# Kernel optimization log

Measured on AMD Instinct MI355X. Metric: run time of the kernel, lower is better.

The kernel has to match this reference:

```python
import jax, jax.numpy as jnp
import numpy as np

IN_FEATURES = 1024
OUT_FEATURES = 64
DEGREE = 3
NUM_KNOTS = 10
BATCH = 8192
K0 = NUM_KNOTS + DEGREE  # number of basis columns / control points per edge


def b_spline_basis(x, knots, degree):
    """Vectorized Cox-de Boor recursion.
    x: (..., ) values in [0,1]; knots: (K0+1,).
    Returns (..., K0) basis; last `degree` columns are zero-padded (matches
    control_points width of num_knots+degree as in the original module).
    """
    t = knots
    n0 = t.shape[0] - 1  # = K0 degree-0 intervals
    xe = x[..., None]
    basis = ((xe >= t[:-1]) & (xe < t[1:])).astype(x.dtype)  # (..., K0)
    for p in range(1, degree + 1):
        ti = t[: n0 - p]
        tip = t[p:n0]
        ti1 = t[1 : n0 - p + 1]
        tip1 = t[p + 1 : n0 + 1]
        d1 = jnp.where(tip - ti > 0, tip - ti, jnp.ones_like(ti))
        d2 = jnp.where(tip1 - ti1 > 0, tip1 - ti1, jnp.ones_like(ti1))
        left = jnp.where(tip - ti > 0, (xe - ti) / d1, 0.0) * basis[..., : n0 - p]
        right = jnp.where(tip1 - ti1 > 0, (tip1 - xe) / d2, 0.0) * basis[..., 1 : n0 - p + 1]
        new = left + right
        pad = jnp.zeros(x.shape + (p,), x.dtype)
        basis = jnp.concatenate([new, pad], axis=-1)
    return basis


def setup_inputs() -> dict:
    key = jax.random.key(0)
    k1, k2 = jax.random.split(key)
    x = jax.random.uniform(k1, (BATCH, IN_FEATURES), dtype=jnp.float32)
    knots = jnp.linspace(0.0, 1.0, NUM_KNOTS + DEGREE + 1, dtype=jnp.float32)
    control_points = jax.random.normal(k2, (OUT_FEATURES, IN_FEATURES, K0), dtype=jnp.float32)
    return {"x": x, "knots": knots, "control_points": control_points}


def reference(x, knots, control_points):
    # basis: (B, in, K0) computed once per input feature (original recomputes
    # it out_features times inside a double loop -- same math, fused here).
    basis = b_spline_basis(x, knots, DEGREE)
    # outputs[b, o] = sum_j sum_k basis[b, j, k] * control_points[o, j, k]
    return jnp.einsum("bjk,ojk->bo", basis, control_points)
```

## Files before the change

kernel.cpp:

```cpp
#include <hip/hip_runtime.h>
#include <hip/hip_bf16.h>
#include <stdint.h>

#define IN_F   1024
#define OUT_F  64
#define BATCH  8192
#define BM     256
#define NTHR   256
#define JSPLIT 32
#define JPB    (IN_F / JSPLIT)
#define JC     4
#define NCH    (JPB / JC)
#define BT_B   (JC * 2048)
#define TBL_B  (14 * 32 * 48)
#define XSTG_B (BM * JPB * 4)
#define LDS_T  (TBL_B + XSTG_B + 2 * BT_B)
#define OUTSZ  (BATCH * OUT_F)

typedef __attribute__((ext_vector_type(8)))  short short8;
typedef __attribute__((ext_vector_type(16))) float f32x16;

__device__ __forceinline__ void gll16(const void* g, void* l) {
    __builtin_amdgcn_global_load_lds(
        (const __attribute__((address_space(1))) uint32_t*)g,
        (__attribute__((address_space(3))) uint32_t*)l,
        16, 0, 0);
}

__global__ void kan_prep(const float* __restrict__ cp, __hip_bfloat16* __restrict__ bt) {
    int j = blockIdx.x * 4 + (threadIdx.x >> 6);
    int o = threadIdx.x & 63;
    const float* src = cp + ((size_t)o * IN_F + j) * 13;
    float v[16];
#pragma unroll
    for (int k = 0; k < 10; ++k) v[k] = src[k];
#pragma unroll
    for (int k = 10; k < 16; ++k) v[k] = 0.0f;
    __hip_bfloat16* dst = bt + (size_t)j * 1024;
#pragma unroll
    for (int kh = 0; kh < 2; ++kh)
#pragma unroll
        for (int e = 0; e < 8; ++e)
            dst[kh * 512 + o * 8 + e] = __float2bfloat16(v[kh * 8 + e]);
}

template<bool PART>
__launch_bounds__(NTHR, 2)
__global__ void kan_main(const float* __restrict__ x,
                         const __hip_bfloat16* __restrict__ bt,
                         void* __restrict__ outp) {
    __shared__ __attribute__((aligned(16))) char lds[LDS_T];

    const int tid   = threadIdx.x;
    const int w     = tid >> 6;
    const int lane  = tid & 63;
    const int l31   = lane & 31;
    const int khalf = lane >> 5;

    const int r0 = blockIdx.x * BM;
    const int j0 = blockIdx.y * JPB;

    const char* btg = (const char*)bt + (size_t)j0 * 2048 + (size_t)tid * 16;
    const char* xgt = (const char*)(x + (size_t)(r0 + tid) * IN_F + j0);
    const int   wofs = w << 10;

#pragma unroll
    for (int p = 0; p < JPB / 4; ++p)
        gll16(xgt + p * 16, lds + TBL_B + p * 4096 + wofs);

#define STAGE_BT(ch, bi) do {                                     \
        char* base_ = lds + TBL_B + XSTG_B + (bi) * BT_B;         \
        const char* gb_ = btg + (size_t)(ch) * BT_B;              \
        gll16(gb_,        base_ + wofs);                          \
        gll16(gb_ + 4096, base_ + 4096 + wofs);                   \
    } while (0)

    STAGE_BT(0, 0);
    STAGE_BT(1, 1);

    for (int e = tid; e < 14 * 32; e += NTHR) {
        const int m = e >> 5, u5 = e & 31;
        const float uu = (u5 + 0.5f) * (1.0f / 32.0f);
        const float u2 = uu * uu;
        const float omu = 1.0f - uu;
        const float o2 = omu * omu;
        const float B3 = u2 * (uu * (1.0f / 6.0f));
        const float B0 = o2 * (omu * (1.0f / 6.0f));
        const float B1 = __builtin_fmaf(u2, __builtin_fmaf(uu, 0.5f, -1.0f), 2.0f / 3.0f);
        const float B2 = 1.0f - B0 - B1 - B3;
        uint32_t P01, P23;
        asm("v_cvt_pk_bf16_f32 %0, %1, %2" : "=v"(P01) : "v"(B0), "v"(B1));
        asm("v_cvt_pk_bf16_f32 %0, %1, %2" : "=v"(P23) : "v"(B2), "v"(B3));
        const uint64_t V = ((uint64_t)P23 << 32) | (uint64_t)P01;
#pragma unroll
        for (int h = 0; h < 2; ++h) {
            const int c0 = 48 + (h << 7);
            const int p = (m << 4) - c0;
            const uint64_t sl = V << ((uint32_t)p & 63);
            const uint64_t sr = V >> ((uint32_t)(-p) & 63);
            const uint64_t t0 = (p < 0) ? sr : sl;
            const uint64_t q0 = ((uint32_t)(p + 63) < 127u) ? t0 : 0ull;
            const uint64_t t1 = (p < 64) ? sr : sl;
            const uint64_t q1 = ((uint32_t)(p - 16) < 112u) ? t1 : 0ull;
            uint64_t* d = (uint64_t*)(lds + e * 48 + h * 16);
            d[0] = q0; d[1] = q1;
        }
    }

#define AFRAG(xv) ({                                              \
        const float t416_ = (xv) * 416.0f;           \
        const int i_ = (int)t416_;                 \
        const int s_ = ((i_ << 1) + i_) << 4;         \
        *(const short8*)(lds + s_ + (khalf << 4)); })

#define COMPUTE(ch, bi) do {                                                  \
        const char* base = lds + TBL_B + XSTG_B + (bi) * BT_B;                \
        float xa0[4], xa1[4];                                                 \
        const char* xr = lds + TBL_B + (ch) * 4096 + (((w << 6) + l31) << 4); \
        *(float4*)xa0 = *(const float4*)(xr);              \
        *(float4*)xa1 = *(const float4*)(xr + 512);     \
        const char* bbb = base + (khalf << 10) + l31 * 16;                    \
        _Pragma("unroll")                                                     \
        for (int jl = 0; jl < JC; ++jl) {                                     \
            const short8 b0 = *(const short8*)(bbb + jl * 2048);              \
            const short8 b1 = *(const short8*)(bbb + jl * 2048 + 512);        \
            const short8 a0 = AFRAG(xa0[jl]);                                 \
            const short8 a1 = AFRAG(xa1[jl]);                                 \
            acc00 = __builtin_amdgcn_mfma_f32_32x32x16_bf16(a0, b0, acc00, 0, 0, 0); \
            acc01 = __builtin_amdgcn_mfma_f32_32x32x16_bf16(a0, b1, acc01, 0, 0, 0); \
            acc10 = __builtin_amdgcn_mfma_f32_32x32x16_bf16(a1, b0, acc10, 0, 0, 0); \
            acc11 = __builtin_amdgcn_mfma_f32_32x32x16_bf16(a1, b1, acc11, 0, 0, 0); \
        }                                                                     \
    } while (0)

    f32x16 acc00, acc01, acc10, acc11;
#pragma unroll
    for (int i = 0; i < 16; ++i) {
        acc00[i] = 0.0f; acc01[i] = 0.0f; acc10[i] = 0.0f; acc11[i] = 0.0f;
    }

    __syncthreads();

    int cur = 0;
#pragma unroll 1
    for (int ch = 0; ch < NCH; ++ch) {
        if (ch >= 2) {
            asm volatile("s_waitcnt vmcnt(2)" ::: "memory");
            __builtin_amdgcn_s_barrier();
            __builtin_amdgcn_sched_barrier(0);
        }
        COMPUTE(ch, cur);
        if (ch + 2 < NCH) {
            __builtin_amdgcn_s_barrier();
            __builtin_amdgcn_sched_barrier(0);
            STAGE_BT(ch + 2, cur);
        }
        cur ^= 1;
    }
#undef STAGE_BT
#undef AFRAG
#undef COMPUTE

    if (PART) {
        __hip_bfloat16* op = (__hip_bfloat16*)outp + (size_t)blockIdx.y * OUTSZ;
#pragma unroll
        for (int r = 0; r < 16; ++r) {
            const int crow = (r & 3) + 8 * (r >> 2) + 4 * khalf;
            __hip_bfloat16* p0 = op + (size_t)(r0 + (w << 6) + crow) * OUT_F;
            __hip_bfloat16* p1 = p0 + 32 * OUT_F;
            p0[l31]      = __float2bfloat16(acc00[r]);
            p0[l31 + 32] = __float2bfloat16(acc01[r]);
            p1[l31]      = __float2bfloat16(acc10[r]);
            p1[l31 + 32] = __float2bfloat16(acc11[r]);
        }
    } else {
        float* op = (float*)outp;
#pragma unroll
        for (int r = 0; r < 16; ++r) {
            const int crow = (r & 3) + 8 * (r >> 2) + 4 * khalf;
            float* p0 = op + (size_t)(r0 + (w << 6) + crow) * OUT_F;
            float* p1 = p0 + 32 * OUT_F;
            atomicAdd(p0 + l31,      acc00[r]);
            atomicAdd(p0 + l31 + 32, acc01[r]);
            atomicAdd(p1 + l31,      acc10[r]);
            atomicAdd(p1 + l31 + 32, acc11[r]);
        }
    }
}

__global__ void kan_reduce(const __hip_bfloat16* __restrict__ part,
                           float* __restrict__ out) {
    const int i = (blockIdx.x * 256 + threadIdx.x) * 8;
    float s[8] = {0, 0, 0, 0, 0, 0, 0, 0};
#pragma unroll
    for (int b = 0; b < JSPLIT; ++b) {
        const short8 v = *(const short8*)(part + (size_t)b * OUTSZ + i);
#pragma unroll
        for (int e = 0; e < 8; ++e) {
            union { uint32_t u; float f; } c;
            c.u = ((uint32_t)(uint16_t)v[e]) << 16;
            s[e] += c.f;
        }
    }
    float4 lo = {s[0], s[1], s[2], s[3]}, hi = {s[4], s[5], s[6], s[7]};
    *(float4*)(out + i)     = lo;
    *(float4*)(out + i + 4) = hi;
}

extern "C" void kernel_launch(void* const* d_in, const int* in_sizes, int n_in,
                              void* d_out, int out_size, void* d_ws, size_t ws_size,
                              hipStream_t stream) {
    const float* x  = (const float*)d_in[0];
    const float* cp = (const float*)d_in[2];
    float* out = (float*)d_out;
    __hip_bfloat16* bt   = (__hip_bfloat16*)d_ws;
    __hip_bfloat16* part = (__hip_bfloat16*)((char*)d_ws + 2u * 1024u * 1024u);

    const size_t need = 2u * 1024u * 1024u + (size_t)JSPLIT * OUTSZ * 2u;
    const bool use_part = ws_size >= need;

    kan_prep<<<dim3(IN_F / 4), dim3(256), 0, stream>>>(cp, bt);
    if (use_part) {
        kan_main<true><<<dim3(BATCH / BM, JSPLIT), dim3(NTHR), 0, stream>>>(x, bt, (void*)part);
        kan_reduce<<<dim3(OUTSZ / 2048), dim3(256), 0, stream>>>(part, out);
    } else {
        hipMemsetAsync(d_out, 0, (size_t)out_size * sizeof(float), stream);
        kan_main<false><<<dim3(BATCH / BM, JSPLIT), dim3(NTHR), 0, stream>>>(x, bt, (void*)d_out);
    }
}
```

Baseline: 42.71 us.

## Halve J split and stage x in two halves with staggered LDS reads

Each block now covers 64 input features instead of 32, halving the number of partial-sum slabs that must be written and reduced. To keep the LDS footprint unchanged, x is staged in two 32-feature halves, with the second half loaded after chunk 7 and the waitcnt logic adjusted for it. The per-wave j order inside a chunk is rotated to reduce LDS bank conflicts, and s_setprio raises wave priority during the MFMA loop. The cost is fewer blocks, so less parallelism, plus an extra synchronization point and more complex vmcnt accounting.

```diff
diff --git a/kernel.cpp b/kernel.cpp
--- a/kernel.cpp
+++ b/kernel.cpp
@@ -7,13 +7,13 @@
 #define BATCH  8192
 #define BM     256
 #define NTHR   256
-#define JSPLIT 32
+#define JSPLIT 16
 #define JPB    (IN_F / JSPLIT)
 #define JC     4
 #define NCH    (JPB / JC)
 #define BT_B   (JC * 2048)
 #define TBL_B  (14 * 32 * 48)
-#define XSTG_B (BM * JPB * 4)
+#define XSTG_B (BM * 32 * 4)
 #define LDS_T  (TBL_B + XSTG_B + 2 * BT_B)
 #define OUTSZ  (BATCH * OUT_F)
 
@@ -64,9 +64,12 @@
     const char* xgt = (const char*)(x + (size_t)(r0 + tid) * IN_F + j0);
     const int   wofs = w << 10;
 
-#pragma unroll
-    for (int p = 0; p < JPB / 4; ++p)
-        gll16(xgt + p * 16, lds + TBL_B + p * 4096 + wofs);
+#define XSTAGE(h) do {                                            \
+        _Pragma("unroll")                                         \
+        for (int p = 0; p < 8; ++p)                               \
+            gll16(xgt + (h) * 128 + p * 16,                       \
+                  lds + TBL_B + p * 4096 + wofs);                 \
+    } while (0)
 
 #define STAGE_BT(ch, bi) do {                                     \
         char* base_ = lds + TBL_B + XSTG_B + (bi) * BT_B;         \
@@ -75,6 +78,7 @@
         gll16(gb_ + 4096, base_ + 4096 + wofs);                   \
     } while (0)
 
+    XSTAGE(0);
     STAGE_BT(0, 0);
     STAGE_BT(1, 1);
 
@@ -116,12 +120,14 @@
 #define COMPUTE(ch, bi) do {                                                  \
         const char* base = lds + TBL_B + XSTG_B + (bi) * BT_B;                \
         float xa0[4], xa1[4];                                                 \
-        const char* xr = lds + TBL_B + (ch) * 4096 + (((w << 6) + l31) << 4); \
+        const char* xr = lds + TBL_B + ((ch) & 7) * 4096 + (((w << 6) + l31) << 4); \
         *(float4*)xa0 = *(const float4*)(xr);              \
         *(float4*)xa1 = *(const float4*)(xr + 512);     \
         const char* bbb = base + (khalf << 10) + l31 * 16;                    \
+        __builtin_amdgcn_s_setprio(1);                                        \
         _Pragma("unroll")                                                     \
-        for (int jl = 0; jl < JC; ++jl) {                                     \
+        for (int jj = 0; jj < JC; ++jj) {                                     \
+            const int jl = (jj + w) & 3;                                      \
             const short8 b0 = *(const short8*)(bbb + jl * 2048);              \
             const short8 b1 = *(const short8*)(bbb + jl * 2048 + 512);        \
             const short8 a0 = AFRAG(xa0[jl]);                                 \
@@ -131,6 +137,7 @@
             acc10 = __builtin_amdgcn_mfma_f32_32x32x16_bf16(a1, b0, acc10, 0, 0, 0); \
             acc11 = __builtin_amdgcn_mfma_f32_32x32x16_bf16(a1, b1, acc11, 0, 0, 0); \
         }                                                                     \
+        __builtin_amdgcn_s_setprio(0);                                        \
     } while (0)
 
     f32x16 acc00, acc01, acc10, acc11;
@@ -144,19 +151,22 @@
     int cur = 0;
 #pragma unroll 1
     for (int ch = 0; ch < NCH; ++ch) {
-        if (ch >= 2) {
-            asm volatile("s_waitcnt vmcnt(2)" ::: "memory");
+        if (ch > 0) {
+            if (ch == NCH - 1) asm volatile("s_waitcnt vmcnt(0)" ::: "memory");
+            else               asm volatile("s_waitcnt vmcnt(2)" ::: "memory");
             __builtin_amdgcn_s_barrier();
             __builtin_amdgcn_sched_barrier(0);
         }
         COMPUTE(ch, cur);
-        if (ch + 2 < NCH) {
+        if (ch + 2 < NCH || ch == 7) {
             __builtin_amdgcn_s_barrier();
             __builtin_amdgcn_sched_barrier(0);
-            STAGE_BT(ch + 2, cur);
+            if (ch == 7) XSTAGE(1);
+            if (ch + 2 < NCH) STAGE_BT(ch + 2, cur);
         }
         cur ^= 1;
     }
+#undef XSTAGE
 #undef STAGE_BT
 #undef AFRAG
 #undef COMPUTE
```

New measurement: 51.91 us. 1.22x slower.

## Use 512 threads per block with 32 rows per wave

Applied to the files above, without the earlier changes.

Doubles the block to 8 waves, so each wave computes a 32x64 output tile with two accumulators instead of a 64x64 tile with four. The x staging and B-tile staging loads are remapped so each thread issues one load per chunk, and the vmcnt waits are adjusted to match. The aim is lower register pressure and higher occupancy (launch bounds now request 4 blocks), giving more latency hiding. The cost is that each A-fragment lookup now feeds only two MFMAs instead of four, and each barrier synchronises more waves.

```diff
diff --git a/kernel.cpp b/kernel.cpp
--- a/kernel.cpp
+++ b/kernel.cpp
@@ -6,7 +6,7 @@
 #define OUT_F  64
 #define BATCH  8192
 #define BM     256
-#define NTHR   256
+#define NTHR   512
 #define JSPLIT 32
 #define JPB    (IN_F / JSPLIT)
 #define JC     4
@@ -45,7 +45,7 @@
 }
 
 template<bool PART>
-__launch_bounds__(NTHR, 2)
+__launch_bounds__(NTHR, 4)
 __global__ void kan_main(const float* __restrict__ x,
                          const __hip_bfloat16* __restrict__ bt,
                          void* __restrict__ outp) {
@@ -61,19 +61,16 @@
     const int j0 = blockIdx.y * JPB;
 
     const char* btg = (const char*)bt + (size_t)j0 * 2048 + (size_t)tid * 16;
-    const char* xgt = (const char*)(x + (size_t)(r0 + tid) * IN_F + j0);
+    const char* xlg = (const char*)x + ((size_t)(r0 + lane) * IN_F + j0) * 4;
     const int   wofs = w << 10;
 
 #pragma unroll
-    for (int p = 0; p < JPB / 4; ++p)
-        gll16(xgt + p * 16, lds + TBL_B + p * 4096 + wofs);
-
-#define STAGE_BT(ch, bi) do {                                     \
-        char* base_ = lds + TBL_B + XSTG_B + (bi) * BT_B;         \
-        const char* gb_ = btg + (size_t)(ch) * BT_B;              \
-        gll16(gb_,        base_ + wofs);                          \
-        gll16(gb_ + 4096, base_ + 4096 + wofs);                   \
-    } while (0)
+    for (int i = 0; i < 4; ++i)
+        gll16(xlg + (size_t)(i * 64) * 4096 + w * 16,
+              lds + TBL_B + (w << 12) + (i << 10));
+
+#define STAGE_BT(ch, bi) \
+    gll16(btg + (size_t)(ch) * BT_B, lds + TBL_B + XSTG_B + (bi) * BT_B + wofs)
 
     STAGE_BT(0, 0);
     STAGE_BT(1, 1);
@@ -115,29 +112,23 @@
 
 #define COMPUTE(ch, bi) do {                                                  \
         const char* base = lds + TBL_B + XSTG_B + (bi) * BT_B;                \
-        float xa0[4], xa1[4];                                                 \
-        const char* xr = lds + TBL_B + (ch) * 4096 + (((w << 6) + l31) << 4); \
-        *(float4*)xa0 = *(const float4*)(xr);              \
-        *(float4*)xa1 = *(const float4*)(xr + 512);     \
+        float xa[4];                                                          \
+        const char* xr = lds + TBL_B + (ch) * 4096 + (((w << 5) + l31) << 4); \
+        *(float4*)xa = *(const float4*)(xr);    \
         const char* bbb = base + (khalf << 10) + l31 * 16;                    \
         _Pragma("unroll")                                                     \
         for (int jl = 0; jl < JC; ++jl) {                                     \
             const short8 b0 = *(const short8*)(bbb + jl * 2048);              \
             const short8 b1 = *(const short8*)(bbb + jl * 2048 + 512);        \
-            const short8 a0 = AFRAG(xa0[jl]);                                 \
-            const short8 a1 = AFRAG(xa1[jl]);                                 \
-            acc00 = __builtin_amdgcn_mfma_f32_32x32x16_bf16(a0, b0, acc00, 0, 0, 0); \
-            acc01 = __builtin_amdgcn_mfma_f32_32x32x16_bf16(a0, b1, acc01, 0, 0, 0); \
-            acc10 = __builtin_amdgcn_mfma_f32_32x32x16_bf16(a1, b0, acc10, 0, 0, 0); \
-            acc11 = __builtin_amdgcn_mfma_f32_32x32x16_bf16(a1, b1, acc11, 0, 0, 0); \
+            const short8 a  = AFRAG(xa[jl]);                                  \
+            acc0 = __builtin_amdgcn_mfma_f32_32x32x16_bf16(a, b0, acc0, 0, 0, 0); \
+            acc1 = __builtin_amdgcn_mfma_f32_32x32x16_bf16(a, b1, acc1, 0, 0, 0); \
         }                                                                     \
     } while (0)
 
-    f32x16 acc00, acc01, acc10, acc11;
-#pragma unroll
-    for (int i = 0; i < 16; ++i) {
-        acc00[i] = 0.0f; acc01[i] = 0.0f; acc10[i] = 0.0f; acc11[i] = 0.0f;
-    }
+    f32x16 acc0, acc1;
+#pragma unroll
+    for (int i = 0; i < 16; ++i) { acc0[i] = 0.0f; acc1[i] = 0.0f; }
 
     __syncthreads();
 
@@ -145,7 +136,8 @@
 #pragma unroll 1
     for (int ch = 0; ch < NCH; ++ch) {
         if (ch >= 2) {
-            asm volatile("s_waitcnt vmcnt(2)" ::: "memory");
+            if (ch == NCH - 1) asm volatile("s_waitcnt vmcnt(0)" ::: "memory");
+            else               asm volatile("s_waitcnt vmcnt(1)" ::: "memory");
             __builtin_amdgcn_s_barrier();
             __builtin_amdgcn_sched_barrier(0);
         }
@@ -166,24 +158,18 @@
 #pragma unroll
         for (int r = 0; r < 16; ++r) {
             const int crow = (r & 3) + 8 * (r >> 2) + 4 * khalf;
-            __hip_bfloat16* p0 = op + (size_t)(r0 + (w << 6) + crow) * OUT_F;
-            __hip_bfloat16* p1 = p0 + 32 * OUT_F;
-            p0[l31]      = __float2bfloat16(acc00[r]);
-            p0[l31 + 32] = __float2bfloat16(acc01[r]);
-            p1[l31]      = __float2bfloat16(acc10[r]);
-            p1[l31 + 32] = __float2bfloat16(acc11[r]);
+            __hip_bfloat16* p0 = op + (size_t)(r0 + (w << 5) + crow) * OUT_F;
+            p0[l31]      = __float2bfloat16(acc0[r]);
+            p0[l31 + 32] = __float2bfloat16(acc1[r]);
         }
     } else {
         float* op = (float*)outp;
 #pragma unroll
         for (int r = 0; r < 16; ++r) {
             const int crow = (r & 3) + 8 * (r >> 2) + 4 * khalf;
-            float* p0 = op + (size_t)(r0 + (w << 6) + crow) * OUT_F;
-            float* p1 = p0 + 32 * OUT_F;
-            atomicAdd(p0 + l31,      acc00[r]);
-            atomicAdd(p0 + l31 + 32, acc01[r]);
-            atomicAdd(p1 + l31,      acc10[r]);
-            atomicAdd(p1 + l31 + 32, acc11[r]);
+            float* p0 = op + (size_t)(r0 + (w << 5) + crow) * OUT_F;
+            atomicAdd(p0 + l31,      acc0[r]);
+            atomicAdd(p0 + l31 + 32, acc1[r]);
         }
     }
 }
```

Measured after the change: 41.02 us. 4.0% less time.
